# Kernel optimization log

Measured on AMD Instinct MI355X. Metric: run time of the kernel, lower is better.

Reference implementation:

```python
import jax, jax.numpy as jnp
import numpy as np

IN_FEATURES = 2048
OUT_FEATURES = 2048
LOG_DIM = 11                      # ceil(log2(2048))
BUTTERFLY_DIM = 2 ** LOG_DIM      # 2048
MAX_BLOCKS = BUTTERFLY_DIM // 2   # 1024 (layer 0 has the most blocks)
BATCH = 16384


def setup_inputs() -> dict:
    key = jax.random.key(0)
    ks = jax.random.split(key, 5)
    x = jax.random.normal(ks[0], (BATCH, IN_FEATURES), dtype=jnp.float32)
    # Linear weights stored torch-style: [out, in]
    w_in = jax.random.normal(ks[1], (BUTTERFLY_DIM, IN_FEATURES), dtype=jnp.float32) * 0.02
    w_out = jax.random.normal(ks[2], (OUT_FEATURES, BUTTERFLY_DIM), dtype=jnp.float32) * 0.02
    b_out = jnp.zeros((OUT_FEATURES,), dtype=jnp.float32)
    # Per-stage rotation params: theta = rand*0.01, a=cos(theta), b=sin(theta).
    # Stage l uses num_blocks = BUTTERFLY_DIM // 2^(l+1) entries; pad to MAX_BLOCKS.
    theta = jax.random.uniform(ks[3], (LOG_DIM, MAX_BLOCKS), dtype=jnp.float32) * 0.01
    a_pad = jnp.cos(theta)
    b_pad = jnp.sin(theta)
    return {"x": x, "w_in": w_in, "w_out": w_out, "b_out": b_out,
            "a_pad": a_pad, "b_pad": b_pad}


def _butterfly(x, a_pad, b_pad):
    # x: [B, BUTTERFLY_DIM]
    B = x.shape[0]
    for l in range(LOG_DIM):
        block_size = 2 ** l
        num_blocks = BUTTERFLY_DIM // (2 * block_size)
        a = a_pad[l, :num_blocks][None, :, None]  # [1, nb, 1]
        b = b_pad[l, :num_blocks][None, :, None]
        xv = x.reshape(B, num_blocks, 2, block_size)
        x0 = xv[:, :, 0, :]
        x1 = xv[:, :, 1, :]
        top = a * x0 + b * x1
        bot = -b * x0 + a * x1
        x = jnp.stack([top, bot], axis=2).reshape(B, BUTTERFLY_DIM)
    return x


def reference(x, w_in, w_out, b_out, a_pad, b_pad):
    h = x @ w_in.T                      # [B, BUTTERFLY_DIM]
    h = _butterfly(h, a_pad, b_pad)
    return h @ w_out.T + b_out          # [B, OUT_FEATURES]
```

## Files before the change

kernel.cpp:

```cpp
#include <hip/hip_runtime.h>
#include <hip/hip_bf16.h>

using bf16 = __hip_bfloat16;
using bf16x8 = __attribute__((ext_vector_type(8))) __bf16;
using f32x4 = __attribute__((ext_vector_type(4))) float;

typedef const __attribute__((address_space(1))) void* gas_ptr;
typedef __attribute__((address_space(3))) void* las_ptr;
#define LOAD_LDS16(g, l) \
    __builtin_amdgcn_global_load_lds((gas_ptr)(const void*)(g), (las_ptr)(void*)(l), 16, 0, 0)

#define LOG_DIM 11
#define BDIM 2048
#define NFEAT 2048
#define BATCH 16384

__global__ __launch_bounds__(256) void prep1(const float* __restrict__ w_out,
                                             const float* __restrict__ a_pad,
                                             const float* __restrict__ b_pad,
                                             const float* __restrict__ w_in,
                                             bf16* __restrict__ woutb,
                                             bf16* __restrict__ wint) {
    __shared__ float v[BDIM];
    __shared__ float tile[32][33];
    const int t = threadIdx.x;
    if (blockIdx.x < 2048) {
        const int o = blockIdx.x;
        const float* row = w_out + (size_t)o * BDIM;
        for (int i = t; i < BDIM / 4; i += 256)
            ((float4*)v)[i] = ((const float4*)row)[i];
        __syncthreads();
        for (int l = LOG_DIM - 1; l >= 0; --l) {
            #pragma unroll
            for (int pp = 0; pp < 4; ++pp) {
                int p = t + pp * 256;
                int j = p >> l;
                int s = p & ((1 << l) - 1);
                int i0 = (j << (l + 1)) | s;
                int i1 = i0 + (1 << l);
                float a = a_pad[l * (BDIM / 2) + j];
                float b = b_pad[l * (BDIM / 2) + j];
                float x0 = v[i0], x1 = v[i1];
                v[i0] = a * x0 - b * x1;
                v[i1] = b * x0 + a * x1;
            }
            __syncthreads();
        }
        union { bf16 h[8]; int4 vv; } u;
        #pragma unroll
        for (int j = 0; j < 8; ++j) u.h[j] = __float2bfloat16(v[t * 8 + j]);
        *(int4*)(woutb + (size_t)o * BDIM + t * 8) = u.vv;
    } else {
        const int b = blockIdx.x - 2048;
        const int bx = b & 63, by = b >> 6;
        const int tx = t & 31, ty = t >> 5;
        #pragma unroll
        for (int r = ty; r < 32; r += 8)
            tile[r][tx] = w_in[(size_t)(by * 32 + r) * NFEAT + bx * 32 + tx];
        __syncthreads();
        #pragma unroll
        for (int r = ty; r < 32; r += 8)
            wint[(size_t)(bx * 32 + r) * NFEAT + by * 32 + tx] = __float2bfloat16(tile[tx][r]);
    }
}

__global__ __launch_bounds__(256, 2) void prep2(const bf16* __restrict__ Aw,
                                                const bf16* __restrict__ Btw,
                                                bf16* __restrict__ Cpart,
                                                const float* __restrict__ x,
                                                bf16* __restrict__ x_bf) {
    __shared__ bf16 sA[128 * 32];
    __shared__ bf16 sB[128 * 32];
    const int tid = threadIdx.x;

    if (blockIdx.x & 1) {
        const int vb = blockIdx.x >> 1;
        #pragma unroll
        for (int it = 0; it < 16; ++it) {
            size_t i = ((size_t)vb * 16 + it) * 2048 + tid * 8;
            float4 v0 = *(const float4*)(x + i);
            float4 v1 = *(const float4*)(x + i + 4);
            union { bf16 h[8]; int4 v; } u;
            u.h[0] = __float2bfloat16(v0.x); u.h[1] = __float2bfloat16(v0.y);
            u.h[2] = __float2bfloat16(v0.z); u.h[3] = __float2bfloat16(v0.w);
            u.h[4] = __float2bfloat16(v1.x); u.h[5] = __float2bfloat16(v1.y);
            u.h[6] = __float2bfloat16(v1.z); u.h[7] = __float2bfloat16(v1.w);
            *(int4*)(x_bf + i) = u.v;
        }
        return;
    }

    constexpr int BK = 32, LDA = 2048, KLEN = 512, NN = 2048;
    const int sk = blockIdx.x >> 1;
    const int bx = sk & 15, by = (sk >> 4) & 15, kz = sk >> 8;
    const bf16* A = Aw + kz * KLEN;
    const bf16* Bt = Btw + kz * KLEN;
    bf16* C = Cpart + (size_t)kz * NN * NN;

    const int wave = tid >> 6, lane = tid & 63;
    const int wr = wave >> 1, wc = wave & 1;
    const int mBase = by * 128, nBase = bx * 128;

    const int r0 = tid >> 2, c0 = tid & 3;
    const int r1 = (256 + tid) >> 2;

    const bf16* gA0 = A + (size_t)(mBase + r0) * LDA + c0 * 8;
    const bf16* gA1 = A + (size_t)(mBase + r1) * LDA + c0 * 8;
    const bf16* gB0 = Bt + (size_t)(nBase + r0) * LDA + c0 * 8;
    const bf16* gB1 = Bt + (size_t)(nBase + r1) * LDA + c0 * 8;

    char* lA0 = (char*)sA + (wave * 64) * 16;
    char* lA1 = (char*)sA + (256 + wave * 64) * 16;
    char* lB0 = (char*)sB + (wave * 64) * 16;
    char* lB1 = (char*)sB + (256 + wave * 64) * 16;

    f32x4 acc[4][4];
    #pragma unroll
    for (int i = 0; i < 4; ++i)
        #pragma unroll
        for (int j = 0; j < 4; ++j) acc[i][j] = (f32x4){0.f, 0.f, 0.f, 0.f};

    const int aRow = wr * 64 + (lane & 15);
    const int bRow = wc * 64 + (lane & 15);
    const int kOff = (lane >> 4) * 8;

    for (int k0 = 0; k0 < KLEN; k0 += BK) {
        LOAD_LDS16(gA0, lA0);
        LOAD_LDS16(gA1, lA1);
        LOAD_LDS16(gB0, lB0);
        LOAD_LDS16(gB1, lB1);
        gA0 += BK; gA1 += BK; gB0 += BK; gB1 += BK;
        __syncthreads();
        bf16x8 af[4], bfr[4];
        #pragma unroll
        for (int mf = 0; mf < 4; ++mf)
            af[mf] = *reinterpret_cast<const bf16x8*>(&sA[(aRow + mf * 16) * BK + kOff]);
        #pragma unroll
        for (int nf = 0; nf < 4; ++nf)
            bfr[nf] = *reinterpret_cast<const bf16x8*>(&sB[(bRow + nf * 16) * BK + kOff]);
        #pragma unroll
        for (int mf = 0; mf < 4; ++mf)
            #pragma unroll
            for (int nf = 0; nf < 4; ++nf)
                acc[mf][nf] = __builtin_amdgcn_mfma_f32_16x16x32_bf16(
                    af[mf], bfr[nf], acc[mf][nf], 0, 0, 0);
        __syncthreads();
    }

    const int cRow0 = mBase + wr * 64 + (lane >> 4) * 4;
    const int cCol0 = nBase + wc * 64 + (lane & 15);
    #pragma unroll
    for (int mf = 0; mf < 4; ++mf)
        #pragma unroll
        for (int nf = 0; nf < 4; ++nf)
            #pragma unroll
            for (int r = 0; r < 4; ++r)
                C[(size_t)(cRow0 + mf * 16 + r) * NN + cCol0 + nf * 16] =
                    __float2bfloat16(acc[mf][nf][r]);
}

__global__ __launch_bounds__(256) void addcvt4(const bf16* __restrict__ p,
                                               bf16* __restrict__ out) {
    size_t i = ((size_t)blockIdx.x * 256 + threadIdx.x) * 8;
    constexpr size_t STRIDE = (size_t)2048 * 2048;
    float s[8];
    #pragma unroll
    for (int j = 0; j < 8; ++j) s[j] = 0.f;
    #pragma unroll
    for (int z = 0; z < 4; ++z) {
        union { bf16 h[8]; int4 v; } a;
        a.v = *(const int4*)(p + z * STRIDE + i);
        #pragma unroll
        for (int j = 0; j < 8; ++j) s[j] += __bfloat162float(a.h[j]);
    }
    union { bf16 h[8]; int4 v; } o;
    #pragma unroll
    for (int j = 0; j < 8; ++j) o.h[j] = __float2bfloat16(s[j]);
    *(int4*)(out + i) = o.v;
}

#define GK 2048
#define LDS_SLOT 65536
#define LDS_BOFF 32768
#define LDS_KH 16384

__global__ __launch_bounds__(512, 2) void gemm256(const bf16* __restrict__ A,
                                                  const bf16* __restrict__ Bt,
                                                  const float* __restrict__ bias,
                                                  float* __restrict__ C) {
    __shared__ __align__(16) char lds[131072];

    const int tid = threadIdx.x;
    const int wave = tid >> 6, lane = tid & 63;
    const int l15 = lane & 15, kc = lane >> 4;
    const int wm = wave >> 2, wn = wave & 3;

    const int bid = blockIdx.x;
    const int swz = (bid & 7) * 64 + (bid >> 3);
    const int bm = swz >> 3, bn = swz & 7;
    const int mBase = bm * 256, nBase = bn * 256;

    const int c_log = tid ^ ((tid >> 3) & 3);
    const int srow = c_log >> 2, skc = c_log & 3;
    const bf16* gA = A + (size_t)(mBase + srow) * GK + skc * 8;
    const bf16* gB = Bt + (size_t)(nBase + srow) * GK + skc * 8;
    const int stgBase = wave * 1024;

    const int kcx = kc ^ ((l15 >> 1) & 3);
    const int aoff = wm * 8192 + l15 * 64 + kcx * 16;
    const int boff = LDS_BOFF + wn * 4096 + l15 * 64 + kcx * 16;

    f32x4 acc[8][4];
    #pragma unroll
    for (int i = 0; i < 8; ++i)
        #pragma unroll
        for (int j = 0; j < 4; ++j) acc[i][j] = (f32x4){0.f, 0.f, 0.f, 0.f};

    bf16x8 Aa[4], Ab[4], Ba[4], Bb[4];

#define STG(GSRC, LDSC, KT, KH) do {                                        \
    const bf16* _g = (GSRC) + (KT) * 64 + (KH) * 32;                        \
    LOAD_LDS16(_g, lds + (LDSC) + stgBase);                                 \
    LOAD_LDS16(_g + (size_t)128 * GK, lds + (LDSC) + stgBase + 8192);       \
} while (0)

#define READP(AN, BN, SLOT, KH, MH, DOB) do {                               \
    const int _rb = (SLOT) * LDS_SLOT + (KH) * LDS_KH;                      \
    _Pragma("unroll")                                                       \
    for (int _f = 0; _f < 4; ++_f)                                          \
        AN[_f] = *(const bf16x8*)(lds + _rb + aoff + (MH) * 4096 + _f * 1024); \
    if (DOB) {                                                              \
        _Pragma("unroll")                                                   \
        for (int _f = 0; _f < 4; ++_f)                                      \
            BN[_f] = *(const bf16x8*)(lds + _rb + boff + _f * 1024);        \
    }                                                                       \
} while (0)

    STG(gA, 0 * LDS_SLOT + 0, 0, 0);
    STG(gB, 0 * LDS_SLOT + LDS_BOFF + 0, 0, 0);
    STG(gA, 0 * LDS_SLOT + LDS_KH, 0, 1);
    STG(gB, 0 * LDS_SLOT + LDS_BOFF + LDS_KH, 0, 1);
    STG(gA, 1 * LDS_SLOT + 0, 1, 0);
    STG(gB, 1 * LDS_SLOT + LDS_BOFF + 0, 1, 0);
    STG(gB, 1 * LDS_SLOT + LDS_BOFF + LDS_KH, 1, 1);
    asm volatile("s_waitcnt vmcnt(6)");
    __builtin_amdgcn_s_barrier();
    READP(Aa, Ba, 0, 0, 0, 1);

#define PH(CURA, CURB, NXTA, NXTB, MH, RS, RKH, RMH, RDOB, SGSRC, SLDS, SKT, SKH, DOVM) do { \
    STG(SGSRC, SLDS, SKT, SKH);                                             \
    if (DOVM) asm volatile("s_waitcnt vmcnt(6)");                           \
    __builtin_amdgcn_s_barrier();                                           \
    READP(NXTA, NXTB, RS, RKH, RMH, RDOB);                                  \
    __builtin_amdgcn_s_setprio(1);                                          \
    _Pragma("unroll")                                                       \
    for (int _mf = 0; _mf < 4; ++_mf)                                       \
        _Pragma("unroll")                                                   \
        for (int _nf = 0; _nf < 4; ++_nf)                                   \
            acc[(MH) * 4 + _mf][_nf] = __builtin_amdgcn_mfma_f32_16x16x32_bf16( \
                CURA[_mf], CURB[_nf], acc[(MH) * 4 + _mf][_nf], 0, 0, 0);   \
    __builtin_amdgcn_s_setprio(0);                                          \
    __builtin_amdgcn_s_barrier();                                           \
} while (0)

    for (int it = 0; it < 16; ++it) {
        const int t0 = 2 * it;
        const int t1 = (t0 + 1) & 31, t2 = (t0 + 2) & 31, t3 = (t0 + 3) & 31;
        PH(Aa, Ba, Ab, Bb, 0, 0, 0, 1, 0, gA, 1 * LDS_SLOT + LDS_KH,            t1, 1, 0);
        PH(Ab, Ba, Aa, Bb, 1, 0, 1, 0, 1, gB, 0 * LDS_SLOT + LDS_BOFF,          t2, 0, 0);
        PH(Aa, Bb, Ab, Ba, 0, 0, 1, 1, 0, gA, 0 * LDS_SLOT + 0,                 t2, 0, 0);
        PH(Ab, Bb, Aa, Ba, 1, 1, 0, 0, 1, gB, 0 * LDS_SLOT + LDS_BOFF + LDS_KH, t2, 1, 1);
        PH(Aa, Ba, Ab, Bb, 0, 1, 0, 1, 0, gA, 0 * LDS_SLOT + LDS_KH,            t2, 1, 0);
        PH(Ab, Ba, Aa, Bb, 1, 1, 1, 0, 1, gB, 1 * LDS_SLOT + LDS_BOFF,          t3, 0, 0);
        PH(Aa, Bb, Ab, Ba, 0, 1, 1, 1, 0, gA, 1 * LDS_SLOT + 0,                 t3, 0, 0);
        PH(Ab, Bb, Aa, Ba, 1, 0, 0, 0, 1, gB, 1 * LDS_SLOT + LDS_BOFF + LDS_KH, t3, 1, 1);
    }

    const int cRow0 = mBase + wm * 128 + (lane >> 4) * 4;
    const int cCol0 = nBase + wn * 64 + l15;
    float bv[4];
    #pragma unroll
    for (int nf = 0; nf < 4; ++nf) bv[nf] = bias[cCol0 + nf * 16];
    #pragma unroll
    for (int Mf = 0; Mf < 8; ++Mf)
        #pragma unroll
        for (int nf = 0; nf < 4; ++nf)
            #pragma unroll
            for (int r = 0; r < 4; ++r)
                C[(size_t)(cRow0 + Mf * 16 + r) * GK + cCol0 + nf * 16] =
                    acc[Mf][nf][r] + bv[nf];
#undef PH
#undef READP
#undef STG
}

extern "C" void kernel_launch(void* const* d_in, const int* in_sizes, int n_in,
                              void* d_out, int out_size, void* d_ws, size_t ws_size,
                              hipStream_t stream) {
    const float* x     = (const float*)d_in[0];
    const float* w_in  = (const float*)d_in[1];
    const float* w_out = (const float*)d_in[2];
    const float* b_out = (const float*)d_in[3];
    const float* a_pad = (const float*)d_in[4];
    const float* b_pad = (const float*)d_in[5];
    float* out = (float*)d_out;

    char* ws = (char*)d_ws;
    bf16* x_bf  = (bf16*)ws;
    bf16* woutb = (bf16*)(ws + (size_t)67108864);
    bf16* wint  = (bf16*)(ws + (size_t)75497472);
    bf16* mcomb = (bf16*)(ws + (size_t)83886080);

    bf16* part = (bf16*)d_out;

    prep1<<<dim3(6144), dim3(256), 0, stream>>>(w_out, a_pad, b_pad, w_in, woutb, wint);
    prep2<<<dim3(2048), dim3(256), 0, stream>>>(woutb, wint, part, x, x_bf);
    addcvt4<<<dim3(NFEAT * BDIM / (256 * 8)), dim3(256), 0, stream>>>(part, mcomb);
    gemm256<<<dim3((BATCH / 256) * (NFEAT / 256)), dim3(512), 0, stream>>>(
        x_bf, mcomb, b_out, out);
}
```

Before: 205.7 us.

## Rebalance x conversion across prep kernels and simplify main GEMM phase pipeline

The x fp32-to-bf16 conversion is split so that 256 chunks run inside prep1 alongside the weight preparation and the remaining 768 chunks run as separate blocks in prep2, replacing the previous interleaving with GEMM blocks. The main 256x256 GEMM loop is restructured from eight half-tile phases with double-buffered register fragments to four phases, each loading a full A and B k-slice and issuing 32 MFMAs. This reduces barrier count and bookkeeping but loses register-level prefetch overlap of LDS reads with MFMAs, and raises register pressure by holding eight A fragments at once.

```diff
diff --git a/kernel.cpp b/kernel.cpp
--- a/kernel.cpp
+++ b/kernel.cpp
@@ -14,13 +14,31 @@
 #define BDIM 2048
 #define NFEAT 2048
 #define BATCH 16384
+
+__device__ __forceinline__ void cvt_chunk(const float* __restrict__ x,
+                                          bf16* __restrict__ x_bf, int chunk, int tid) {
+    #pragma unroll
+    for (int it = 0; it < 16; ++it) {
+        size_t i = ((size_t)chunk * 16 + it) * 2048 + tid * 8;
+        float4 v0 = *(const float4*)(x + i);
+        float4 v1 = *(const float4*)(x + i + 4);
+        union { bf16 h[8]; int4 v; } u;
+        u.h[0] = __float2bfloat16(v0.x); u.h[1] = __float2bfloat16(v0.y);
+        u.h[2] = __float2bfloat16(v0.z); u.h[3] = __float2bfloat16(v0.w);
+        u.h[4] = __float2bfloat16(v1.x); u.h[5] = __float2bfloat16(v1.y);
+        u.h[6] = __float2bfloat16(v1.z); u.h[7] = __float2bfloat16(v1.w);
+        *(int4*)(x_bf + i) = u.v;
+    }
+}
 
 __global__ __launch_bounds__(256) void prep1(const float* __restrict__ w_out,
                                              const float* __restrict__ a_pad,
                                              const float* __restrict__ b_pad,
                                              const float* __restrict__ w_in,
                                              bf16* __restrict__ woutb,
-                                             bf16* __restrict__ wint) {
+                                             bf16* __restrict__ wint,
+                                             const float* __restrict__ x,
+                                             bf16* __restrict__ x_bf) {
     __shared__ float v[BDIM];
     __shared__ float tile[32][33];
     const int t = threadIdx.x;
@@ -50,7 +68,7 @@
         #pragma unroll
         for (int j = 0; j < 8; ++j) u.h[j] = __float2bfloat16(v[t * 8 + j]);
         *(int4*)(woutb + (size_t)o * BDIM + t * 8) = u.vv;
-    } else {
+    } else if (blockIdx.x < 6144) {
         const int b = blockIdx.x - 2048;
         const int bx = b & 63, by = b >> 6;
         const int tx = t & 31, ty = t >> 5;
@@ -61,6 +79,8 @@
         #pragma unroll
         for (int r = ty; r < 32; r += 8)
             wint[(size_t)(bx * 32 + r) * NFEAT + by * 32 + tx] = __float2bfloat16(tile[tx][r]);
+    } else {
+        cvt_chunk(x, x_bf, 768 + (blockIdx.x - 6144), t);
     }
 }
 
@@ -73,25 +93,13 @@
     __shared__ bf16 sB[128 * 32];
     const int tid = threadIdx.x;
 
-    if (blockIdx.x & 1) {
-        const int vb = blockIdx.x >> 1;
-        #pragma unroll
-        for (int it = 0; it < 16; ++it) {
-            size_t i = ((size_t)vb * 16 + it) * 2048 + tid * 8;
-            float4 v0 = *(const float4*)(x + i);
-            float4 v1 = *(const float4*)(x + i + 4);
-            union { bf16 h[8]; int4 v; } u;
-            u.h[0] = __float2bfloat16(v0.x); u.h[1] = __float2bfloat16(v0.y);
-            u.h[2] = __float2bfloat16(v0.z); u.h[3] = __float2bfloat16(v0.w);
-            u.h[4] = __float2bfloat16(v1.x); u.h[5] = __float2bfloat16(v1.y);
-            u.h[6] = __float2bfloat16(v1.z); u.h[7] = __float2bfloat16(v1.w);
-            *(int4*)(x_bf + i) = u.v;
-        }
+    if (blockIdx.x >= 1024) {
+        cvt_chunk(x, x_bf, blockIdx.x - 1024, tid);
         return;
     }
 
     constexpr int BK = 32, LDA = 2048, KLEN = 512, NN = 2048;
-    const int sk = blockIdx.x >> 1;
+    const int sk = blockIdx.x;
     const int bx = sk & 15, by = (sk >> 4) & 15, kz = sk >> 8;
     const bf16* A = Aw + kz * KLEN;
     const bf16* Bt = Btw + kz * KLEN;
@@ -216,24 +224,34 @@
         #pragma unroll
         for (int j = 0; j < 4; ++j) acc[i][j] = (f32x4){0.f, 0.f, 0.f, 0.f};
 
-    bf16x8 Aa[4], Ab[4], Ba[4], Bb[4];
-
 #define STG(GSRC, LDSC, KT, KH) do {                                        \
     const bf16* _g = (GSRC) + (KT) * 64 + (KH) * 32;                        \
     LOAD_LDS16(_g, lds + (LDSC) + stgBase);                                 \
     LOAD_LDS16(_g + (size_t)128 * GK, lds + (LDSC) + stgBase + 8192);       \
 } while (0)
 
-#define READP(AN, BN, SLOT, KH, MH, DOB) do {                               \
-    const int _rb = (SLOT) * LDS_SLOT + (KH) * LDS_KH;                      \
+#define PH(S, KH, SA_LDS, SB_LDS, SKT, SKH) do {                            \
+    STG(gA, SA_LDS, SKT, SKH);                                              \
+    STG(gB, SB_LDS, SKT, SKH);                                              \
+    asm volatile("s_waitcnt vmcnt(8)");                                     \
+    __builtin_amdgcn_s_barrier();                                           \
+    const int _rb = (S) * LDS_SLOT + (KH) * LDS_KH;                         \
+    bf16x8 _a[8], _b[4];                                                    \
+    _Pragma("unroll")                                                       \
+    for (int _f = 0; _f < 8; ++_f)                                          \
+        _a[_f] = *(const bf16x8*)(lds + _rb + aoff + _f * 1024);            \
     _Pragma("unroll")                                                       \
     for (int _f = 0; _f < 4; ++_f)                                          \
-        AN[_f] = *(const bf16x8*)(lds + _rb + aoff + (MH) * 4096 + _f * 1024); \
-    if (DOB) {                                                              \
+        _b[_f] = *(const bf16x8*)(lds + _rb + boff + _f * 1024);            \
+    __builtin_amdgcn_s_setprio(1);                                          \
+    _Pragma("unroll")                                                       \
+    for (int _mf = 0; _mf < 8; ++_mf)                                       \
         _Pragma("unroll")                                                   \
-        for (int _f = 0; _f < 4; ++_f)                                      \
-            BN[_f] = *(const bf16x8*)(lds + _rb + boff + _f * 1024);        \
-    }                                                                       \
+        for (int _nf = 0; _nf < 4; ++_nf)                                   \
+            acc[_mf][_nf] = __builtin_amdgcn_mfma_f32_16x16x32_bf16(        \
+                _a[_mf], _b[_nf], acc[_mf][_nf], 0, 0, 0);                  \
+    __builtin_amdgcn_s_setprio(0);                                          \
+    __builtin_amdgcn_s_barrier();                                           \
 } while (0)
 
     STG(gA, 0 * LDS_SLOT + 0, 0, 0);
@@ -242,38 +260,14 @@
     STG(gB, 0 * LDS_SLOT + LDS_BOFF + LDS_KH, 0, 1);
     STG(gA, 1 * LDS_SLOT + 0, 1, 0);
     STG(gB, 1 * LDS_SLOT + LDS_BOFF + 0, 1, 0);
-    STG(gB, 1 * LDS_SLOT + LDS_BOFF + LDS_KH, 1, 1);
-    asm volatile("s_waitcnt vmcnt(6)");
-    __builtin_amdgcn_s_barrier();
-    READP(Aa, Ba, 0, 0, 0, 1);
-
-#define PH(CURA, CURB, NXTA, NXTB, MH, RS, RKH, RMH, RDOB, SGSRC, SLDS, SKT, SKH, DOVM) do { \
-    STG(SGSRC, SLDS, SKT, SKH);                                             \
-    if (DOVM) asm volatile("s_waitcnt vmcnt(6)");                           \
-    __builtin_amdgcn_s_barrier();                                           \
-    READP(NXTA, NXTB, RS, RKH, RMH, RDOB);                                  \
-    __builtin_amdgcn_s_setprio(1);                                          \
-    _Pragma("unroll")                                                       \
-    for (int _mf = 0; _mf < 4; ++_mf)                                       \
-        _Pragma("unroll")                                                   \
-        for (int _nf = 0; _nf < 4; ++_nf)                                   \
-            acc[(MH) * 4 + _mf][_nf] = __builtin_amdgcn_mfma_f32_16x16x32_bf16( \
-                CURA[_mf], CURB[_nf], acc[(MH) * 4 + _mf][_nf], 0, 0, 0);   \
-    __builtin_amdgcn_s_setprio(0);                                          \
-    __builtin_amdgcn_s_barrier();                                           \
-} while (0)
 
     for (int it = 0; it < 16; ++it) {
         const int t0 = 2 * it;
         const int t1 = (t0 + 1) & 31, t2 = (t0 + 2) & 31, t3 = (t0 + 3) & 31;
-        PH(Aa, Ba, Ab, Bb, 0, 0, 0, 1, 0, gA, 1 * LDS_SLOT + LDS_KH,            t1, 1, 0);
-        PH(Ab, Ba, Aa, Bb, 1, 0, 1, 0, 1, gB, 0 * LDS_SLOT + LDS_BOFF,          t2, 0, 0);
-        PH(Aa, Bb, Ab, Ba, 0, 0, 1, 1, 0, gA, 0 * LDS_SLOT + 0,                 t2, 0, 0);
-        PH(Ab, Bb, Aa, Ba, 1, 1, 0, 0, 1, gB, 0 * LDS_SLOT + LDS_BOFF + LDS_KH, t2, 1, 1);
-        PH(Aa, Ba, Ab, Bb, 0, 1, 0, 1, 0, gA, 0 * LDS_SLOT + LDS_KH,            t2, 1, 0);
-        PH(Ab, Ba, Aa, Bb, 1, 1, 1, 0, 1, gB, 1 * LDS_SLOT + LDS_BOFF,          t3, 0, 0);
-        PH(Aa, Bb, Ab, Ba, 0, 1, 1, 1, 0, gA, 1 * LDS_SLOT + 0,                 t3, 0, 0);
-        PH(Ab, Bb, Aa, Ba, 1, 0, 0, 0, 1, gB, 1 * LDS_SLOT + LDS_BOFF + LDS_KH, t3, 1, 1);
+        PH(0, 0, 1 * LDS_SLOT + LDS_KH, 1 * LDS_SLOT + LDS_BOFF + LDS_KH, t1, 1);
+        PH(0, 1, 0 * LDS_SLOT + 0,      0 * LDS_SLOT + LDS_BOFF,          t2, 0);
+        PH(1, 0, 0 * LDS_SLOT + LDS_KH, 0 * LDS_SLOT + LDS_BOFF + LDS_KH, t2, 1);
+        PH(1, 1, 1 * LDS_SLOT + 0,      1 * LDS_SLOT + LDS_BOFF,          t3, 0);
     }
 
     const int cRow0 = mBase + wm * 128 + (lane >> 4) * 4;
@@ -290,7 +284,6 @@
                 C[(size_t)(cRow0 + Mf * 16 + r) * GK + cCol0 + nf * 16] =
                     acc[Mf][nf][r] + bv[nf];
 #undef PH
-#undef READP
 #undef STG
 }
 
@@ -313,8 +306,9 @@
 
     bf16* part = (bf16*)d_out;
 
-    prep1<<<dim3(6144), dim3(256), 0, stream>>>(w_out, a_pad, b_pad, w_in, woutb, wint);
-    prep2<<<dim3(2048), dim3(256), 0, stream>>>(woutb, wint, part, x, x_bf);
+    prep1<<<dim3(6400), dim3(256), 0, stream>>>(w_out, a_pad, b_pad, w_in,
+                                                woutb, wint, x, x_bf);
+    prep2<<<dim3(1792), dim3(256), 0, stream>>>(woutb, wint, part, x, x_bf);
     addcvt4<<<dim3(NFEAT * BDIM / (256 * 8)), dim3(256), 0, stream>>>(part, mcomb);
     gemm256<<<dim3((BATCH / 256) * (NFEAT / 256)), dim3(512), 0, stream>>>(
         x_bf, mcomb, b_out, out);
```

After: 232.6 us. +13.1%, slower.

## Switch main GEMM to 32x32x16 MFMA and rebalance x conversion across prep kernels

Applied to the files above, without the earlier changes.

The main GEMM's inner product moves from 16x16x32 to 32x32x16 bf16 MFMA instructions. LDS fragment reads and the epilogue's accumulator-to-output index mapping change to match, and the XOR swizzle is kept. Separately, the x fp32-to-bf16 conversion is split: 256 chunks move into prep1 and 768 stay in prep2, which no longer interleaves conversion blocks with its split-K GEMM blocks. The larger MFMA issues fewer instructions per unit of work, and the rebalancing evens out prep kernel durations, at the cost of a more complex accumulator layout.

```diff
diff --git a/kernel.cpp b/kernel.cpp
--- a/kernel.cpp
+++ b/kernel.cpp
@@ -4,6 +4,7 @@
 using bf16 = __hip_bfloat16;
 using bf16x8 = __attribute__((ext_vector_type(8))) __bf16;
 using f32x4 = __attribute__((ext_vector_type(4))) float;
+using f32x16 = __attribute__((ext_vector_type(16))) float;
 
 typedef const __attribute__((address_space(1))) void* gas_ptr;
 typedef __attribute__((address_space(3))) void* las_ptr;
@@ -14,13 +15,31 @@
 #define BDIM 2048
 #define NFEAT 2048
 #define BATCH 16384
+
+__device__ __forceinline__ void cvt_chunk(const float* __restrict__ x,
+                                          bf16* __restrict__ x_bf, int chunk, int tid) {
+    #pragma unroll
+    for (int it = 0; it < 16; ++it) {
+        size_t i = ((size_t)chunk * 16 + it) * 2048 + tid * 8;
+        float4 v0 = *(const float4*)(x + i);
+        float4 v1 = *(const float4*)(x + i + 4);
+        union { bf16 h[8]; int4 v; } u;
+        u.h[0] = __float2bfloat16(v0.x); u.h[1] = __float2bfloat16(v0.y);
+        u.h[2] = __float2bfloat16(v0.z); u.h[3] = __float2bfloat16(v0.w);
+        u.h[4] = __float2bfloat16(v1.x); u.h[5] = __float2bfloat16(v1.y);
+        u.h[6] = __float2bfloat16(v1.z); u.h[7] = __float2bfloat16(v1.w);
+        *(int4*)(x_bf + i) = u.v;
+    }
+}
 
 __global__ __launch_bounds__(256) void prep1(const float* __restrict__ w_out,
                                              const float* __restrict__ a_pad,
                                              const float* __restrict__ b_pad,
                                              const float* __restrict__ w_in,
                                              bf16* __restrict__ woutb,
-                                             bf16* __restrict__ wint) {
+                                             bf16* __restrict__ wint,
+                                             const float* __restrict__ x,
+                                             bf16* __restrict__ x_bf) {
     __shared__ float v[BDIM];
     __shared__ float tile[32][33];
     const int t = threadIdx.x;
@@ -50,7 +69,7 @@
         #pragma unroll
         for (int j = 0; j < 8; ++j) u.h[j] = __float2bfloat16(v[t * 8 + j]);
         *(int4*)(woutb + (size_t)o * BDIM + t * 8) = u.vv;
-    } else {
+    } else if (blockIdx.x < 6144) {
         const int b = blockIdx.x - 2048;
         const int bx = b & 63, by = b >> 6;
         const int tx = t & 31, ty = t >> 5;
@@ -61,6 +80,8 @@
         #pragma unroll
         for (int r = ty; r < 32; r += 8)
             wint[(size_t)(bx * 32 + r) * NFEAT + by * 32 + tx] = __float2bfloat16(tile[tx][r]);
+    } else {
+        cvt_chunk(x, x_bf, 768 + (blockIdx.x - 6144), t);
     }
 }
 
@@ -73,25 +94,13 @@
     __shared__ bf16 sB[128 * 32];
     const int tid = threadIdx.x;
 
-    if (blockIdx.x & 1) {
-        const int vb = blockIdx.x >> 1;
-        #pragma unroll
-        for (int it = 0; it < 16; ++it) {
-            size_t i = ((size_t)vb * 16 + it) * 2048 + tid * 8;
-            float4 v0 = *(const float4*)(x + i);
-            float4 v1 = *(const float4*)(x + i + 4);
-            union { bf16 h[8]; int4 v; } u;
-            u.h[0] = __float2bfloat16(v0.x); u.h[1] = __float2bfloat16(v0.y);
-            u.h[2] = __float2bfloat16(v0.z); u.h[3] = __float2bfloat16(v0.w);
-            u.h[4] = __float2bfloat16(v1.x); u.h[5] = __float2bfloat16(v1.y);
-            u.h[6] = __float2bfloat16(v1.z); u.h[7] = __float2bfloat16(v1.w);
-            *(int4*)(x_bf + i) = u.v;
-        }
+    if (blockIdx.x >= 1024) {
+        cvt_chunk(x, x_bf, blockIdx.x - 1024, tid);
         return;
     }
 
     constexpr int BK = 32, LDA = 2048, KLEN = 512, NN = 2048;
-    const int sk = blockIdx.x >> 1;
+    const int sk = blockIdx.x;
     const int bx = sk & 15, by = (sk >> 4) & 15, kz = sk >> 8;
     const bf16* A = Aw + kz * KLEN;
     const bf16* Bt = Btw + kz * KLEN;
@@ -192,7 +201,7 @@
 
     const int tid = threadIdx.x;
     const int wave = tid >> 6, lane = tid & 63;
-    const int l15 = lane & 15, kc = lane >> 4;
+    const int l31 = lane & 31, hi = lane >> 5;
     const int wm = wave >> 2, wn = wave & 3;
 
     const int bid = blockIdx.x;
@@ -206,15 +215,19 @@
     const bf16* gB = Bt + (size_t)(nBase + srow) * GK + skc * 8;
     const int stgBase = wave * 1024;
 
-    const int kcx = kc ^ ((l15 >> 1) & 3);
-    const int aoff = wm * 8192 + l15 * 64 + kcx * 16;
-    const int boff = LDS_BOFF + wn * 4096 + l15 * 64 + kcx * 16;
-
-    f32x4 acc[8][4];
-    #pragma unroll
-    for (int i = 0; i < 8; ++i)
-        #pragma unroll
-        for (int j = 0; j < 4; ++j) acc[i][j] = (f32x4){0.f, 0.f, 0.f, 0.f};
+    const int sx = (l31 >> 1) & 3;
+    const int sl0 = (hi ^ sx) << 4;
+    const int sl1 = ((2 | hi) ^ sx) << 4;
+    const int rowA = (wm * 128 + l31) * 64;
+    const int rowB = LDS_BOFF + (wn * 64 + l31) * 64;
+
+    f32x16 acc[4][2];
+    #pragma unroll
+    for (int i = 0; i < 4; ++i)
+        #pragma unroll
+        for (int j = 0; j < 2; ++j)
+            #pragma unroll
+            for (int r = 0; r < 16; ++r) acc[i][j][r] = 0.f;
 
     bf16x8 Aa[4], Ab[4], Ba[4], Bb[4];
 
@@ -227,12 +240,16 @@
 #define READP(AN, BN, SLOT, KH, MH, DOB) do {                               \
     const int _rb = (SLOT) * LDS_SLOT + (KH) * LDS_KH;                      \
     _Pragma("unroll")                                                       \
-    for (int _f = 0; _f < 4; ++_f)                                          \
-        AN[_f] = *(const bf16x8*)(lds + _rb + aoff + (MH) * 4096 + _f * 1024); \
+    for (int _mb = 0; _mb < 2; ++_mb) {                                     \
+        AN[_mb * 2 + 0] = *(const bf16x8*)(lds + _rb + rowA + ((MH) * 2 + _mb) * 2048 + sl0); \
+        AN[_mb * 2 + 1] = *(const bf16x8*)(lds + _rb + rowA + ((MH) * 2 + _mb) * 2048 + sl1); \
+    }                                                                       \
     if (DOB) {                                                              \
         _Pragma("unroll")                                                   \
-        for (int _f = 0; _f < 4; ++_f)                                      \
-            BN[_f] = *(const bf16x8*)(lds + _rb + boff + _f * 1024);        \
+        for (int _nb = 0; _nb < 2; ++_nb) {                                 \
+            BN[_nb * 2 + 0] = *(const bf16x8*)(lds + _rb + rowB + _nb * 2048 + sl0); \
+            BN[_nb * 2 + 1] = *(const bf16x8*)(lds + _rb + rowB + _nb * 2048 + sl1); \
+        }                                                                   \
     }                                                                       \
 } while (0)
 
@@ -254,11 +271,14 @@
     READP(NXTA, NXTB, RS, RKH, RMH, RDOB);                                  \
     __builtin_amdgcn_s_setprio(1);                                          \
     _Pragma("unroll")                                                       \
-    for (int _mf = 0; _mf < 4; ++_mf)                                       \
+    for (int _ks = 0; _ks < 2; ++_ks)                                       \
         _Pragma("unroll")                                                   \
-        for (int _nf = 0; _nf < 4; ++_nf)                                   \
-            acc[(MH) * 4 + _mf][_nf] = __builtin_amdgcn_mfma_f32_16x16x32_bf16( \
-                CURA[_mf], CURB[_nf], acc[(MH) * 4 + _mf][_nf], 0, 0, 0);   \
+        for (int _mb = 0; _mb < 2; ++_mb)                                   \
+            _Pragma("unroll")                                               \
+            for (int _nb = 0; _nb < 2; ++_nb)                               \
+                acc[(MH) * 2 + _mb][_nb] = __builtin_amdgcn_mfma_f32_32x32x16_bf16( \
+                    CURA[_mb * 2 + _ks], CURB[_nb * 2 + _ks],               \
+                    acc[(MH) * 2 + _mb][_nb], 0, 0, 0);                     \
     __builtin_amdgcn_s_setprio(0);                                          \
     __builtin_amdgcn_s_barrier();                                           \
 } while (0)
@@ -276,19 +296,20 @@
         PH(Ab, Bb, Aa, Ba, 1, 0, 0, 0, 1, gB, 1 * LDS_SLOT + LDS_BOFF + LDS_KH, t3, 1, 1);
     }
 
-    const int cRow0 = mBase + wm * 128 + (lane >> 4) * 4;
-    const int cCol0 = nBase + wn * 64 + l15;
-    float bv[4];
-    #pragma unroll
-    for (int nf = 0; nf < 4; ++nf) bv[nf] = bias[cCol0 + nf * 16];
-    #pragma unroll
-    for (int Mf = 0; Mf < 8; ++Mf)
-        #pragma unroll
-        for (int nf = 0; nf < 4; ++nf)
-            #pragma unroll
-            for (int r = 0; r < 4; ++r)
-                C[(size_t)(cRow0 + Mf * 16 + r) * GK + cCol0 + nf * 16] =
-                    acc[Mf][nf][r] + bv[nf];
+    #pragma unroll
+    for (int mb = 0; mb < 4; ++mb) {
+        #pragma unroll
+        for (int nb = 0; nb < 2; ++nb) {
+            const int col = nBase + wn * 64 + nb * 32 + l31;
+            const float bv = bias[col];
+            const int rbase = mBase + wm * 128 + mb * 32 + 4 * hi;
+            #pragma unroll
+            for (int r = 0; r < 16; ++r) {
+                const int row = rbase + (r & 3) + 8 * (r >> 2);
+                C[(size_t)row * GK + col] = acc[mb][nb][r] + bv;
+            }
+        }
+    }
 #undef PH
 #undef READP
 #undef STG
@@ -313,8 +334,9 @@
 
     bf16* part = (bf16*)d_out;
 
-    prep1<<<dim3(6144), dim3(256), 0, stream>>>(w_out, a_pad, b_pad, w_in, woutb, wint);
-    prep2<<<dim3(2048), dim3(256), 0, stream>>>(woutb, wint, part, x, x_bf);
+    prep1<<<dim3(6400), dim3(256), 0, stream>>>(w_out, a_pad, b_pad, w_in,
+                                                woutb, wint, x, x_bf);
+    prep2<<<dim3(1792), dim3(256), 0, stream>>>(woutb, wint, part, x, x_bf);
     addcvt4<<<dim3(NFEAT * BDIM / (256 * 8)), dim3(256), 0, stream>>>(part, mcomb);
     gemm256<<<dim3((BATCH / 256) * (NFEAT / 256)), dim3(512), 0, stream>>>(
         x_bf, mcomb, b_out, out);
```

Measured after the change: 238.1 us. 1.16x slower.
